# Performance work log

Measured on AMD Instinct MI355X. Metric: run time of the kernel, lower is better.

Reference implementation:

```python
import jax, jax.numpy as jnp
import numpy as np

B, N, D_IN, D_OUT, E = 16, 16384, 128, 128, 65536
LN_EPS = 1e-5


def setup_inputs() -> dict:
    key = jax.random.key(0)
    k1, k2, k3, k4 = jax.random.split(key, 4)
    x = jax.random.normal(k1, (B, N, D_IN), dtype=jnp.float32)
    edge_index = jax.random.randint(k2, (2, E), 0, N, dtype=jnp.int64)
    W_self = jax.random.normal(k3, (D_OUT, D_IN), dtype=jnp.float32) / np.sqrt(D_IN)
    W_neigh = jax.random.normal(k4, (D_OUT, D_IN), dtype=jnp.float32) / np.sqrt(D_IN)
    return {
        "x": x,
        "edge_index": edge_index,
        "batch_size": B,
        "W_self": W_self,
        "W_neigh": W_neigh,
        "bias": jnp.zeros((D_OUT,), jnp.float32),
        "gamma": jnp.ones((D_OUT,), jnp.float32),
        "beta": jnp.zeros((D_OUT,), jnp.float32),
    }


def reference(x, edge_index, batch_size, W_self, W_neigh, bias, gamma, beta):
    b, n, d = x.shape
    src, dst = edge_index[0], edge_index[1]
    # expand edge index for disjoint batched graphs: add per-graph node offsets
    offsets = (jnp.arange(batch_size, dtype=src.dtype) * n)[:, None]  # [B,1]
    src_e = (src[None, :] + offsets).reshape(-1)  # [B*E]
    dst_e = (dst[None, :] + offsets).reshape(-1)
    x_flat = x.reshape(batch_size * n, d)
    # scatter-sum neighbor features and degrees, then mean
    agg = jax.ops.segment_sum(x_flat[src_e], dst_e, num_segments=batch_size * n)
    deg = jax.ops.segment_sum(jnp.ones_like(dst_e, dtype=x_flat.dtype), dst_e,
                              num_segments=batch_size * n)
    neigh = agg / jnp.maximum(deg, 1.0)[:, None]
    out = x_flat @ W_self.T + neigh @ W_neigh.T + bias  # [B*N, D_OUT]
    # LayerNorm over last dim
    mu = jnp.mean(out, axis=-1, keepdims=True)
    var = jnp.mean(jnp.square(out - mu), axis=-1, keepdims=True)
    out = (out - mu) * jax.lax.rsqrt(var + LN_EPS) * gamma + beta
    out = jax.nn.relu(out)
    return out.reshape(batch_size, n, -1)
```

## Files before the change

kernel.cpp:

```cpp
#include <hip/hip_runtime.h>
#include <hip/hip_bf16.h>
#include <stdint.h>

#define B_ 16
#define N_ 16384
#define D_ 128
#define E_ 65536

typedef __attribute__((ext_vector_type(8))) __bf16 bf16x8;
typedef __attribute__((ext_vector_type(4))) float f32x4;

__device__ __forceinline__ uint16_t f2bf(float f) {
    union { float f; uint32_t u; } v;
    v.f = f;
    uint32_t u = v.u;
    uint32_t r = (u + 0x7fffu + ((u >> 16) & 1u)) >> 16;
    return (uint16_t)r;
}

__device__ __forceinline__ bool ei_is64(const int* __restrict__ ei, int t) {
    int w = ei[2 * (t & 63) + 1];
    return __ballot(w != 0) == 0ull;
}

__global__ void k_cntpack(const int* __restrict__ ei,
                          const float* __restrict__ wself,
                          const float* __restrict__ wneigh,
                          int* __restrict__ deg,
                          uint16_t* __restrict__ wpack) {
    int t = threadIdx.x;
    int bid = blockIdx.x;
    if (bid < 256) {
        bool is64 = ei_is64(ei, t);
        int e = bid * 256 + t;
        int d = is64 ? ei[2 * (E_ + e)] : ei[E_ + e];
        atomicAdd(&deg[d], 1);
    } else {
        int g = (bid - 256) * 256 + t;
        int j = g & 7;
        int lane = (g >> 3) & 63;
        int nt = (g >> 9) & 7;
        int ks = g >> 12;
        int k = ks * 32 + (lane >> 4) * 8 + j;
        int n = nt * 16 + (lane & 15);
        float v = (k < 128) ? wself[n * 128 + k] : wneigh[n * 128 + (k - 128)];
        wpack[g] = f2bf(v);
    }
}

__global__ void k_scan(const int* __restrict__ deg, int* __restrict__ off,
                       int* __restrict__ cur) {
    __shared__ int ps[256];
    int t = threadIdx.x;
    int vals[64];
    const int4* dv = (const int4*)(deg + t * 64);
    int s = 0;
#pragma unroll
    for (int i = 0; i < 16; i++) {
        int4 v = dv[i];
        vals[4 * i + 0] = v.x; vals[4 * i + 1] = v.y;
        vals[4 * i + 2] = v.z; vals[4 * i + 3] = v.w;
        s += v.x + v.y + v.z + v.w;
    }
    ps[t] = s;
    __syncthreads();
#pragma unroll
    for (int st = 1; st < 256; st <<= 1) {
        int add = (t >= st) ? ps[t - st] : 0;
        __syncthreads();
        ps[t] += add;
        __syncthreads();
    }
    int run = ps[t] - s;
#pragma unroll
    for (int i = 0; i < 64; i++) {
        off[t * 64 + i] = run;
        cur[t * 64 + i] = run;
        run += vals[i];
    }
    if (t == 255) off[N_] = run;
}

__global__ void k_fill(const int* __restrict__ ei, int* __restrict__ cur,
                       int* __restrict__ adj) {
    int t = threadIdx.x;
    bool is64 = ei_is64(ei, t);
    int e = blockIdx.x * 256 + t;
    int s = is64 ? ei[2 * e] : ei[e];
    int d = is64 ? ei[2 * (E_ + e)] : ei[E_ + e];
    int p = atomicAdd(&cur[d], 1);
    adj[p] = s;
}

__global__ __launch_bounds__(256) void k_agg(const float* __restrict__ x,
                                             const int* __restrict__ off,
                                             const int* __restrict__ adj,
                                             unsigned char* __restrict__ scratch) {
    int t = threadIdx.x;
    int g = blockIdx.x & 15;
    int chunk = blockIdx.x >> 4;
    int hw = t >> 5, l = t & 31;
    int node = chunk * 8 + hw;
    int o0 = off[node], o1 = off[node + 1];
    const float* xg = x + (size_t)g * N_ * D_;
    float ax = 0.f, ay = 0.f, az = 0.f, aw = 0.f;
    int e = o0;
    for (; e + 1 < o1; e += 2) {
        int s0 = adj[e], s1 = adj[e + 1];
        float4 v0 = *(const float4*)(xg + (size_t)s0 * D_ + l * 4);
        float4 v1 = *(const float4*)(xg + (size_t)s1 * D_ + l * 4);
        ax += v0.x + v1.x; ay += v0.y + v1.y;
        az += v0.z + v1.z; aw += v0.w + v1.w;
    }
    if (e < o1) {
        int s0 = adj[e];
        float4 v0 = *(const float4*)(xg + (size_t)s0 * D_ + l * 4);
        ax += v0.x; ay += v0.y; az += v0.z; aw += v0.w;
    }
    float sc = 1.f / fmaxf((float)(o1 - o0), 1.f);
    uint32_t p0 = (uint32_t)f2bf(ax * sc) | ((uint32_t)f2bf(ay * sc) << 16);
    uint32_t p1 = (uint32_t)f2bf(az * sc) | ((uint32_t)f2bf(aw * sc) << 16);
    uint2 pv; pv.x = p0; pv.y = p1;
    *(uint2*)(scratch + ((size_t)g * N_ + node) * 512 + 256 + l * 8) = pv;
}

__global__ __launch_bounds__(256) void k_main(
    const float* __restrict__ x,
    const uint16_t* __restrict__ wpack,
    const float* __restrict__ bias,
    const float* __restrict__ gamma_,
    const float* __restrict__ beta_,
    float* out) {
    __shared__ __align__(16) unsigned char smem[33792];
    __shared__ float prm[3][128];
    uint16_t* As = (uint16_t*)smem;
    float* Cs = (float*)smem;

    int t = threadIdx.x;
    int b = blockIdx.x & 15;
    int tile = blockIdx.x >> 4;
    int node0 = tile * 64;

    if (t < 128) {
        prm[0][t] = bias[t];
        prm[1][t] = gamma_[t];
        prm[2][t] = beta_[t];
    }

    int r = t >> 2;
    int q = t & 3;
    int node = node0 + r;
    const size_t xrow_base = ((size_t)b * N_ + node) * D_;
    int mt = r >> 4, m = r & 15;

    {
        const float4* xv = (const float4*)(x + xrow_base);
#pragma unroll
        for (int c = 0; c < 4; c++) {
            float4 a0 = xv[q * 8 + 2 * c + 0];
            float4 a1 = xv[q * 8 + 2 * c + 1];
            float f[8] = {a0.x, a0.y, a0.z, a0.w, a1.x, a1.y, a1.z, a1.w};
            uint32_t pk[4];
#pragma unroll
            for (int p = 0; p < 4; p++)
                pk[p] = (uint32_t)f2bf(f[2 * p]) | ((uint32_t)f2bf(f[2 * p + 1]) << 16);
            int kc = q * 4 + c;
            int ks = kc >> 2, qd = kc & 3;
            uint4 v = make_uint4(pk[0], pk[1], pk[2], pk[3]);
            *(uint4*)&As[(((ks * 4 + mt) * 64) + qd * 16 + m) * 8] = v;
        }
    }

    {
        const uint4* nv = (const uint4*)((const unsigned char*)out +
                                         ((size_t)b * N_ + node) * 512 + 256);
#pragma unroll
        for (int c = 0; c < 4; c++) {
            uint4 v = nv[q * 4 + c];
            int kc = 16 + q * 4 + c;
            int ks = kc >> 2, qd = kc & 3;
            *(uint4*)&As[(((ks * 4 + mt) * 64) + qd * 16 + m) * 8] = v;
        }
    }

    __syncthreads();

    int wv = t >> 6;
    int lane = t & 63;
    f32x4 accv[4][2];
#pragma unroll
    for (int i = 0; i < 4; i++)
#pragma unroll
        for (int j = 0; j < 2; j++) {
            f32x4 z = {0.f, 0.f, 0.f, 0.f};
            accv[i][j] = z;
        }

    const uint4* wp = (const uint4*)wpack;
#pragma unroll
    for (int ks = 0; ks < 8; ks++) {
        uint4 b0u = wp[(ks * 8 + 2 * wv + 0) * 64 + lane];
        uint4 b1u = wp[(ks * 8 + 2 * wv + 1) * 64 + lane];
        bf16x8 bf0 = __builtin_bit_cast(bf16x8, b0u);
        bf16x8 bf1 = __builtin_bit_cast(bf16x8, b1u);
#pragma unroll
        for (int mtt = 0; mtt < 4; mtt++) {
            bf16x8 a = *(const bf16x8*)&As[((ks * 4 + mtt) * 64 + lane) * 8];
            accv[mtt][0] = __builtin_amdgcn_mfma_f32_16x16x32_bf16(a, bf0, accv[mtt][0], 0, 0, 0);
            accv[mtt][1] = __builtin_amdgcn_mfma_f32_16x16x32_bf16(a, bf1, accv[mtt][1], 0, 0, 0);
        }
    }

    __syncthreads();

#pragma unroll
    for (int mtt = 0; mtt < 4; mtt++)
#pragma unroll
        for (int ntl = 0; ntl < 2; ntl++)
#pragma unroll
            for (int rg = 0; rg < 4; rg++) {
                int row = mtt * 16 + (lane >> 4) * 4 + rg;
                int col = (2 * wv + ntl) * 16 + (lane & 15);
                Cs[row * 132 + (col >> 5) * 33 + (col & 31)] = accv[mtt][ntl][rg];
            }

    __syncthreads();

    {
        float s1 = 0.f, s2 = 0.f;
#pragma unroll
        for (int i = 0; i < 32; i++) {
            float v = Cs[r * 132 + q * 33 + i] + prm[0][q * 32 + i];
            s1 += v;
            s2 += v * v;
        }
        s1 += __shfl_xor(s1, 1, 64);
        s2 += __shfl_xor(s2, 1, 64);
        s1 += __shfl_xor(s1, 2, 64);
        s2 += __shfl_xor(s2, 2, 64);
        float mu = s1 * (1.f / 128.f);
        float var = s2 * (1.f / 128.f) - mu * mu;
        float rstd = rsqrtf(var + 1e-5f);

        float* orow = out + xrow_base;
#pragma unroll
        for (int c = 0; c < 8; c++) {
            float4 o;
            float tmp[4];
#pragma unroll
            for (int j = 0; j < 4; j++) {
                int i0 = c * 4 + j;
                int d0 = q * 32 + i0;
                float v = Cs[r * 132 + q * 33 + i0] + prm[0][d0];
                tmp[j] = fmaxf((v - mu) * rstd * prm[1][d0] + prm[2][d0], 0.f);
            }
            o.x = tmp[0]; o.y = tmp[1]; o.z = tmp[2]; o.w = tmp[3];
            *(float4*)&orow[q * 32 + c * 4] = o;
        }
    }
}

extern "C" void kernel_launch(void* const* d_in, const int* in_sizes, int n_in,
                              void* d_out, int out_size, void* d_ws, size_t ws_size,
                              hipStream_t stream) {
    (void)in_sizes; (void)n_in; (void)out_size; (void)ws_size;
    const float* x      = (const float*)d_in[0];
    const int*   ei     = (const int*)d_in[1];
    const float* wself  = (const float*)d_in[3];
    const float* wneigh = (const float*)d_in[4];
    const float* bias   = (const float*)d_in[5];
    const float* gma    = (const float*)d_in[6];
    const float* bta    = (const float*)d_in[7];
    float* out = (float*)d_out;

    char* ws = (char*)d_ws;
    int* deg        = (int*)(ws);
    int* off        = (int*)(ws + 65536);
    int* cur        = (int*)(ws + 131584);
    int* adj        = (int*)(ws + 197120);
    uint16_t* wpack = (uint16_t*)(ws + 459264);

    hipMemsetAsync(deg, 0, N_ * sizeof(int), stream);
    k_cntpack<<<384, 256, 0, stream>>>(ei, wself, wneigh, deg, wpack);
    k_scan<<<1, 256, 0, stream>>>(deg, off, cur);
    k_fill<<<E_ / 256, 256, 0, stream>>>(ei, cur, adj);
    k_agg<<<B_ * N_ / 8, 256, 0, stream>>>(x, off, adj, (unsigned char*)out);
    k_main<<<B_ * (N_ / 64), 256, 0, stream>>>(x, wpack, bias, gma, bta, out);
}
```

Measured before the change: 389.6 us.

## Fuse neighbor aggregation into main GEMM kernel and gather from fp16 copy of x

Drops the separate aggregation kernel, so each main-kernel block gathers and averages neighbor rows for its 64 nodes straight into shared memory. This removes the bf16 scratch round trip through the output buffer. When workspace is large enough, the pack kernel also writes an fp16 copy of x so the random gathers read half the bytes. In exchange every call pays a full extra pass that reads x and writes the fp16 copy, and fp16 adds a small precision loss.

```diff
diff --git a/kernel.cpp b/kernel.cpp
--- a/kernel.cpp
+++ b/kernel.cpp
@@ -9,6 +9,7 @@
 
 typedef __attribute__((ext_vector_type(8))) __bf16 bf16x8;
 typedef __attribute__((ext_vector_type(4))) float f32x4;
+typedef __attribute__((ext_vector_type(4))) _Float16 half4;
 
 __device__ __forceinline__ uint16_t f2bf(float f) {
     union { float f; uint32_t u; } v;
@@ -26,8 +27,10 @@
 __global__ void k_cntpack(const int* __restrict__ ei,
                           const float* __restrict__ wself,
                           const float* __restrict__ wneigh,
+                          const float* __restrict__ x,
                           int* __restrict__ deg,
-                          uint16_t* __restrict__ wpack) {
+                          uint16_t* __restrict__ wpack,
+                          _Float16* __restrict__ xh) {
     int t = threadIdx.x;
     int bid = blockIdx.x;
     if (bid < 256) {
@@ -35,7 +38,7 @@
         int e = bid * 256 + t;
         int d = is64 ? ei[2 * (E_ + e)] : ei[E_ + e];
         atomicAdd(&deg[d], 1);
-    } else {
+    } else if (bid < 384) {
         int g = (bid - 256) * 256 + t;
         int j = g & 7;
         int lane = (g >> 3) & 63;
@@ -45,6 +48,16 @@
         int n = nt * 16 + (lane & 15);
         float v = (k < 128) ? wself[n * 128 + k] : wneigh[n * 128 + (k - 128)];
         wpack[g] = f2bf(v);
+    } else {
+        size_t idx = (size_t)(bid - 384) * 2048 + (size_t)t * 8;
+        const float4* p = (const float4*)(x + idx);
+        float4 v0 = p[0], v1 = p[1];
+        union { _Float16 h[8]; uint4 u; } pk;
+        pk.h[0] = (_Float16)v0.x; pk.h[1] = (_Float16)v0.y;
+        pk.h[2] = (_Float16)v0.z; pk.h[3] = (_Float16)v0.w;
+        pk.h[4] = (_Float16)v1.x; pk.h[5] = (_Float16)v1.y;
+        pk.h[6] = (_Float16)v1.z; pk.h[7] = (_Float16)v1.w;
+        *(uint4*)(xh + idx) = pk.u;
     }
 }
 
@@ -92,45 +105,17 @@
     adj[p] = s;
 }
 
-__global__ __launch_bounds__(256) void k_agg(const float* __restrict__ x,
-                                             const int* __restrict__ off,
-                                             const int* __restrict__ adj,
-                                             unsigned char* __restrict__ scratch) {
-    int t = threadIdx.x;
-    int g = blockIdx.x & 15;
-    int chunk = blockIdx.x >> 4;
-    int hw = t >> 5, l = t & 31;
-    int node = chunk * 8 + hw;
-    int o0 = off[node], o1 = off[node + 1];
-    const float* xg = x + (size_t)g * N_ * D_;
-    float ax = 0.f, ay = 0.f, az = 0.f, aw = 0.f;
-    int e = o0;
-    for (; e + 1 < o1; e += 2) {
-        int s0 = adj[e], s1 = adj[e + 1];
-        float4 v0 = *(const float4*)(xg + (size_t)s0 * D_ + l * 4);
-        float4 v1 = *(const float4*)(xg + (size_t)s1 * D_ + l * 4);
-        ax += v0.x + v1.x; ay += v0.y + v1.y;
-        az += v0.z + v1.z; aw += v0.w + v1.w;
-    }
-    if (e < o1) {
-        int s0 = adj[e];
-        float4 v0 = *(const float4*)(xg + (size_t)s0 * D_ + l * 4);
-        ax += v0.x; ay += v0.y; az += v0.z; aw += v0.w;
-    }
-    float sc = 1.f / fmaxf((float)(o1 - o0), 1.f);
-    uint32_t p0 = (uint32_t)f2bf(ax * sc) | ((uint32_t)f2bf(ay * sc) << 16);
-    uint32_t p1 = (uint32_t)f2bf(az * sc) | ((uint32_t)f2bf(aw * sc) << 16);
-    uint2 pv; pv.x = p0; pv.y = p1;
-    *(uint2*)(scratch + ((size_t)g * N_ + node) * 512 + 256 + l * 8) = pv;
-}
-
+template <bool USE_H>
 __global__ __launch_bounds__(256) void k_main(
     const float* __restrict__ x,
+    const _Float16* __restrict__ xh,
+    const int* __restrict__ off,
+    const int* __restrict__ adj,
     const uint16_t* __restrict__ wpack,
     const float* __restrict__ bias,
     const float* __restrict__ gamma_,
     const float* __restrict__ beta_,
-    float* out) {
+    float* __restrict__ out) {
     __shared__ __align__(16) unsigned char smem[33792];
     __shared__ float prm[3][128];
     uint16_t* As = (uint16_t*)smem;
@@ -172,14 +157,54 @@
     }
 
     {
-        const uint4* nv = (const uint4*)((const unsigned char*)out +
-                                         ((size_t)b * N_ + node) * 512 + 256);
-#pragma unroll
-        for (int c = 0; c < 4; c++) {
-            uint4 v = nv[q * 4 + c];
-            int kc = 16 + q * 4 + c;
+        int hw = t >> 5, l = t & 31;
+        for (int i = 0; i < 8; i++) {
+            int r2 = hw * 8 + i;
+            int nd = node0 + r2;
+            int o0 = off[nd], o1 = off[nd + 1];
+            float a0 = 0.f, a1 = 0.f, a2 = 0.f, a3 = 0.f;
+            if (USE_H) {
+                const _Float16* xg = xh + (size_t)b * N_ * D_;
+                int e = o0;
+                for (; e + 1 < o1; e += 2) {
+                    int s0 = adj[e], s1 = adj[e + 1];
+                    half4 v0 = *(const half4*)(xg + (size_t)s0 * D_ + l * 4);
+                    half4 v1 = *(const half4*)(xg + (size_t)s1 * D_ + l * 4);
+                    a0 += (float)v0.x + (float)v1.x;
+                    a1 += (float)v0.y + (float)v1.y;
+                    a2 += (float)v0.z + (float)v1.z;
+                    a3 += (float)v0.w + (float)v1.w;
+                }
+                if (e < o1) {
+                    int s0 = adj[e];
+                    half4 v0 = *(const half4*)(xg + (size_t)s0 * D_ + l * 4);
+                    a0 += (float)v0.x; a1 += (float)v0.y;
+                    a2 += (float)v0.z; a3 += (float)v0.w;
+                }
+            } else {
+                const float* xg = x + (size_t)b * N_ * D_;
+                int e = o0;
+                for (; e + 1 < o1; e += 2) {
+                    int s0 = adj[e], s1 = adj[e + 1];
+                    float4 v0 = *(const float4*)(xg + (size_t)s0 * D_ + l * 4);
+                    float4 v1 = *(const float4*)(xg + (size_t)s1 * D_ + l * 4);
+                    a0 += v0.x + v1.x; a1 += v0.y + v1.y;
+                    a2 += v0.z + v1.z; a3 += v0.w + v1.w;
+                }
+                if (e < o1) {
+                    int s0 = adj[e];
+                    float4 v0 = *(const float4*)(xg + (size_t)s0 * D_ + l * 4);
+                    a0 += v0.x; a1 += v0.y; a2 += v0.z; a3 += v0.w;
+                }
+            }
+            float sc = 1.f / fmaxf((float)(o1 - o0), 1.f);
+            int mt2 = r2 >> 4, m2 = r2 & 15;
+            int kc = 16 + (l >> 1);
             int ks = kc >> 2, qd = kc & 3;
-            *(uint4*)&As[(((ks * 4 + mt) * 64) + qd * 16 + m) * 8] = v;
+            uint2 pv;
+            pv.x = (uint32_t)f2bf(a0 * sc) | ((uint32_t)f2bf(a1 * sc) << 16);
+            pv.y = (uint32_t)f2bf(a2 * sc) | ((uint32_t)f2bf(a3 * sc) << 16);
+            *(uint2*)&As[(((ks * 4 + mt2) * 64) + qd * 16 + m2) * 8 + (l & 1) * 4] = pv;
         }
     }
 
@@ -263,7 +288,7 @@
 extern "C" void kernel_launch(void* const* d_in, const int* in_sizes, int n_in,
                               void* d_out, int out_size, void* d_ws, size_t ws_size,
                               hipStream_t stream) {
-    (void)in_sizes; (void)n_in; (void)out_size; (void)ws_size;
+    (void)in_sizes; (void)n_in; (void)out_size;
     const float* x      = (const float*)d_in[0];
     const int*   ei     = (const int*)d_in[1];
     const float* wself  = (const float*)d_in[3];
@@ -279,11 +304,20 @@
     int* cur        = (int*)(ws + 131584);
     int* adj        = (int*)(ws + 197120);
     uint16_t* wpack = (uint16_t*)(ws + 459264);
+    _Float16* xh    = (_Float16*)(ws + 524800);
+
+    bool use_h = d_ws != nullptr &&
+                 ws_size >= (size_t)524800 + (size_t)B_ * N_ * D_ * 2;
 
     hipMemsetAsync(deg, 0, N_ * sizeof(int), stream);
-    k_cntpack<<<384, 256, 0, stream>>>(ei, wself, wneigh, deg, wpack);
+    k_cntpack<<<use_h ? 16768 : 384, 256, 0, stream>>>(ei, wself, wneigh, x, deg,
+                                                       wpack, xh);
     k_scan<<<1, 256, 0, stream>>>(deg, off, cur);
     k_fill<<<E_ / 256, 256, 0, stream>>>(ei, cur, adj);
-    k_agg<<<B_ * N_ / 8, 256, 0, stream>>>(x, off, adj, (unsigned char*)out);
-    k_main<<<B_ * (N_ / 64), 256, 0, stream>>>(x, wpack, bias, gma, bta, out);
-}
+    if (use_h)
+        k_main<true><<<B_ * (N_ / 64), 256, 0, stream>>>(x, xh, off, adj, wpack,
+                                                         bias, gma, bta, out);
+    else
+        k_main<false><<<B_ * (N_ / 64), 256, 0, stream>>>(x, xh, off, adj, wpack,
+                                                          bias, gma, bta, out);
+}
```

New measurement: 427.1 us. 9.6% more time.
